# Performance work log

Measured on AMD Instinct MI355X. Metric: run time of the kernel, lower is better.

Reference implementation:

```python
import jax, jax.numpy as jnp
import numpy as np
import math

B, C, T = 32, 512, 1024
QUERY_DIM = 512
SCALE = 1.0 / math.sqrt(QUERY_DIM)


def setup_inputs() -> dict:
    key = jax.random.key(0)
    ks = jax.random.split(key, 10)
    lim = 1.0 / math.sqrt(C)  # torch Linear default init range
    return {
        "x": jax.random.normal(ks[0], (B, C, T), dtype=jnp.float32),
        "g_query": jax.random.uniform(ks[1], (B, C, T), dtype=jnp.float32),
        "g_keys": jax.random.uniform(ks[2], (B, C, T), dtype=jnp.float32),
        "g_values": jax.random.uniform(ks[3], (B, C, T), dtype=jnp.float32),
        "Wq": jax.random.uniform(ks[4], (C, C), jnp.float32, -lim, lim),
        "bq": jax.random.uniform(ks[5], (C,), jnp.float32, -lim, lim),
        "Wk": jax.random.uniform(ks[6], (C, C), jnp.float32, -lim, lim),
        "bk": jax.random.uniform(ks[7], (C,), jnp.float32, -lim, lim),
        "Wv": jax.random.uniform(ks[8], (C, C), jnp.float32, -lim, lim),
        "bv": jax.random.uniform(ks[9], (C,), jnp.float32, -lim, lim),
    }


def reference(x, g_query, g_keys, g_values, Wq, bq, Wk, bk, Wv, bv):
    # x, gates: [B, C, T] -> transpose to [B, T, C]
    xt = jnp.swapaxes(x, 1, 2)
    gq = jnp.swapaxes(g_query, 1, 2)
    gk = jnp.swapaxes(g_keys, 1, 2)
    gv = jnp.swapaxes(g_values, 1, 2)
    # torch Linear: y = x @ W^T + b
    q = gq * (jnp.einsum('btc,dc->btd', xt, Wq) + bq)  # [B, T, C]
    k = gk * (jnp.einsum('btc,dc->btd', xt, Wk) + bk)  # [B, T, C]
    v = gv * (jnp.einsum('btc,dc->btd', xt, Wv) + bv)  # [B, T, C]
    # energy[b,c,d] = sum_t q[b,t,c] * k[b,t,d]  (channel-channel attention)
    energy = jnp.einsum('btc,btd->bcd', q, k)  # [B, C, C]
    attn = jax.nn.softmax(energy * SCALE, axis=2)
    # out[b,c,t] = sum_d attn[b,c,d] * v[b,t,d]
    out = jnp.einsum('bcd,btd->bct', attn, v)  # [B, C, T]
    return out
```

## Files before the change

kernel.cpp:

```cpp
#include <hip/hip_runtime.h>
#include <math.h>


#define B_ 32
#define C_ 512
#define T_ 1024
#define TC_ ((size_t)524288)
#define CC_ ((size_t)262144)
#define SCALE_ 0.04419417382415922f

typedef short bf16x8 __attribute__((ext_vector_type(8)));
typedef float f32x4 __attribute__((ext_vector_type(4)));

__device__ __forceinline__ unsigned short f2b(float f) {
    unsigned int u = __float_as_uint(f);
    u += 0x7fff + ((u >> 16) & 1);
    return (unsigned short)(u >> 16);
}
__device__ __forceinline__ float b2f(unsigned short h) {
    return __uint_as_float(((unsigned int)h) << 16);
}

#define GLDS(gp, lp) __builtin_amdgcn_global_load_lds( \
    (const __attribute__((address_space(1))) unsigned int*)(const void*)(gp), \
    (__attribute__((address_space(3))) unsigned int*)(void*)(lp), 16, 0, 0)

template<int M, int N, int K, int LD, int EP>
__global__ __launch_bounds__(256, 2) void gemm_nt(
    const unsigned short* __restrict__ Ahi, const unsigned short* __restrict__ Alo, size_t sA,
    const unsigned short* __restrict__ Bhi, const unsigned short* __restrict__ Blo, size_t sB,
    float* __restrict__ Cf, size_t sCf,
    unsigned short* __restrict__ Chi, unsigned short* __restrict__ Clo, size_t sC,
    const float* __restrict__ gate, size_t sG,
    const float* __restrict__ bias)
{
    __shared__ __attribute__((aligned(16))) unsigned short sAh0[128 * 32];
    __shared__ __attribute__((aligned(16))) unsigned short sAl0[128 * 32];
    __shared__ __attribute__((aligned(16))) unsigned short sBh0[128 * 32];
    __shared__ __attribute__((aligned(16))) unsigned short sBl0[128 * 32];
    __shared__ __attribute__((aligned(16))) unsigned short sAh1[128 * 32];
    __shared__ __attribute__((aligned(16))) unsigned short sAl1[128 * 32];
    __shared__ __attribute__((aligned(16))) unsigned short sBh1[128 * 32];
    __shared__ __attribute__((aligned(16))) unsigned short sBl1[128 * 32];

    const int tid  = threadIdx.x;
    const int lane = tid & 63;
    const int wave = tid >> 6;
    const int bz   = (EP == 2) ? (blockIdx.z >> 1) : blockIdx.z;
    const size_t kbase = (EP == 2) ? (size_t)(blockIdx.z & 1) * K : 0;
    const int m0   = blockIdx.y * 128;
    const int n0   = blockIdx.x * 128;

    const unsigned short* pAh = Ahi + (size_t)bz * sA;
    const unsigned short* pAl = Alo + (size_t)bz * sA;
    const unsigned short* pBh = Bhi + (size_t)bz * sB;
    const unsigned short* pBl = Blo + (size_t)bz * sB;

    const int srow = wave * 32;
    const int lr   = lane >> 2;
    const int lk   = (lane & 3) * 8;
    const size_t gA0 = (size_t)(m0 + srow + lr) * LD + lk + kbase;
    const size_t gA1 = (size_t)(m0 + srow + 16 + lr) * LD + lk + kbase;
    const size_t gB0 = (size_t)(n0 + srow + lr) * LD + lk + kbase;
    const size_t gB1 = (size_t)(n0 + srow + 16 + lr) * LD + lk + kbase;

    const int wm = (wave & 1) * 64;
    const int wn = (wave >> 1) * 64;
    const int fr = lane & 15;
    const int fk = (lane >> 4) * 8;

    f32x4 acc[4][4] = {};

#define STAGE(AH, AL, BH, BL, koff) do { \
    GLDS(pAh + gA0 + (koff), &AH[srow * 32]); \
    GLDS(pAh + gA1 + (koff), &AH[(srow + 16) * 32]); \
    GLDS(pAl + gA0 + (koff), &AL[srow * 32]); \
    GLDS(pAl + gA1 + (koff), &AL[(srow + 16) * 32]); \
    GLDS(pBh + gB0 + (koff), &BH[srow * 32]); \
    GLDS(pBh + gB1 + (koff), &BH[(srow + 16) * 32]); \
    GLDS(pBl + gB0 + (koff), &BL[srow * 32]); \
    GLDS(pBl + gB1 + (koff), &BL[(srow + 16) * 32]); \
} while (0)

#define COMPUTE(AH, AL, BH, BL) do { \
    bf16x8 aH[4], aL[4], bH[4], bL[4]; \
    _Pragma("unroll") \
    for (int i = 0; i < 4; ++i) { \
        int ar = (wm + i * 16 + fr) * 32 + fk; \
        int br = (wn + i * 16 + fr) * 32 + fk; \
        aH[i] = *(const bf16x8*)(const void*)&AH[ar]; \
        aL[i] = *(const bf16x8*)(const void*)&AL[ar]; \
        bH[i] = *(const bf16x8*)(const void*)&BH[br]; \
        bL[i] = *(const bf16x8*)(const void*)&BL[br]; \
    } \
    _Pragma("unroll") \
    for (int mi = 0; mi < 4; ++mi) \
        _Pragma("unroll") \
        for (int ni = 0; ni < 4; ++ni) { \
            acc[mi][ni] = __builtin_amdgcn_mfma_f32_16x16x32_bf16(aL[mi], bH[ni], acc[mi][ni], 0, 0, 0); \
            acc[mi][ni] = __builtin_amdgcn_mfma_f32_16x16x32_bf16(aH[mi], bL[ni], acc[mi][ni], 0, 0, 0); \
            acc[mi][ni] = __builtin_amdgcn_mfma_f32_16x16x32_bf16(aH[mi], bH[ni], acc[mi][ni], 0, 0, 0); \
        } \
} while (0)

    STAGE(sAh0, sAl0, sBh0, sBl0, 0);
    __syncthreads();

    for (int k0 = 0; k0 < K; k0 += 64) {
        STAGE(sAh1, sAl1, sBh1, sBl1, k0 + 32);
        COMPUTE(sAh0, sAl0, sBh0, sBl0);
        __syncthreads();
        if (k0 + 64 < K) STAGE(sAh0, sAl0, sBh0, sBl0, k0 + 64);
        COMPUTE(sAh1, sAl1, sBh1, sBl1);
        __syncthreads();
    }

#undef STAGE
#undef COMPUTE

    #pragma unroll
    for (int mi = 0; mi < 4; ++mi) {
        #pragma unroll
        for (int r = 0; r < 4; ++r) {
            int m = m0 + wm + mi * 16 + (lane >> 4) * 4 + r;
            #pragma unroll
            for (int ni = 0; ni < 4; ++ni) {
                int n = n0 + wn + ni * 16 + fr;
                float v = acc[mi][ni][r];
                size_t idx = (size_t)m * N + n;
                if (EP == 0 || EP == 1) {
                    float g = gate[(size_t)bz * sG + idx];
                    float val = g * (v + bias[EP == 0 ? m : n]);
                    unsigned short h = f2b(val);
                    Chi[(size_t)bz * sC + idx] = h;
                    Clo[(size_t)bz * sC + idx] = f2b(val - b2f(h));
                } else if (EP == 2) {
                    Cf[(size_t)blockIdx.z * sCf + idx] = v * SCALE_;
                } else {
                    Cf[(size_t)bz * sCf + idx] = v;
                }
            }
        }
    }
}

__global__ __launch_bounds__(256) void transpose_split(
    const float* __restrict__ x, const float* __restrict__ gv,
    unsigned short* __restrict__ xThi, unsigned short* __restrict__ xTlo,
    float* __restrict__ gvT, int bc, int b_off)
{
    __shared__ float s[64][65];
    const int z = blockIdx.z;
    const int job = z / bc, bz = z % bc;
    const int t0 = blockIdx.x * 64, c0 = blockIdx.y * 64;
    const float* src = (job ? gv : x) + (size_t)(b_off + bz) * TC_;
    const int col = threadIdx.x & 63, rb = threadIdx.x >> 6;

    #pragma unroll
    for (int i = 0; i < 64; i += 4)
        s[i + rb][col] = src[(size_t)(c0 + i + rb) * T_ + t0 + col];
    __syncthreads();

    const size_t ob = (size_t)bz * TC_;
    #pragma unroll
    for (int i = 0; i < 64; i += 4) {
        int tr = i + rb;
        float v = s[col][tr];
        size_t o = ob + (size_t)(t0 + tr) * C_ + c0 + col;
        if (job == 0) {
            unsigned short h = f2b(v);
            xThi[o] = h;
            xTlo[o] = f2b(v - b2f(h));
        } else {
            gvT[o] = v;
        }
    }
}

__global__ __launch_bounds__(256) void split_mat(
    const float* __restrict__ W, unsigned short* __restrict__ hi,
    unsigned short* __restrict__ lo, int n)
{
    int i = blockIdx.x * 256 + threadIdx.x;
    if (i < n) {
        float v = W[i];
        unsigned short h = f2b(v);
        hi[i] = h;
        lo[i] = f2b(v - b2f(h));
    }
}

__global__ __launch_bounds__(256) void softmax_split(
    const float* __restrict__ E, unsigned short* __restrict__ Ahi,
    unsigned short* __restrict__ Alo)
{
    const int row = blockIdx.x;
    const int bz = row >> 9;
    const int c  = row & (C_ - 1);
    const float* p0 = E + (size_t)(2 * bz) * CC_ + (size_t)c * C_;
    const int tid = threadIdx.x;

    float v0 = p0[tid] + p0[CC_ + tid];
    float v1 = p0[tid + 256] + p0[CC_ + tid + 256];
    float m = fmaxf(v0, v1);
    #pragma unroll
    for (int off = 32; off > 0; off >>= 1)
        m = fmaxf(m, __shfl_down(m, off, 64));

    __shared__ float sm[4];
    if ((tid & 63) == 0) sm[tid >> 6] = m;
    __syncthreads();
    float M = fmaxf(fmaxf(sm[0], sm[1]), fmaxf(sm[2], sm[3]));

    float e0 = expf(v0 - M), e1 = expf(v1 - M);
    float s = e0 + e1;
    #pragma unroll
    for (int off = 32; off > 0; off >>= 1)
        s += __shfl_down(s, off, 64);

    __shared__ float ss[4];
    if ((tid & 63) == 0) ss[tid >> 6] = s;
    __syncthreads();
    float inv = 1.0f / (ss[0] + ss[1] + ss[2] + ss[3]);

    float a0 = e0 * inv, a1 = e1 * inv;
    size_t o = (size_t)row * C_ + tid;
    unsigned short h0 = f2b(a0);
    Ahi[o] = h0;  Alo[o] = f2b(a0 - b2f(h0));
    unsigned short h1 = f2b(a1);
    Ahi[o + 256] = h1;  Alo[o + 256] = f2b(a1 - b2f(h1));
}

extern "C" void kernel_launch(void* const* d_in, const int* in_sizes, int n_in,
                              void* d_out, int out_size, void* d_ws, size_t ws_size,
                              hipStream_t stream) {
    const float* x  = (const float*)d_in[0];
    const float* gq = (const float*)d_in[1];
    const float* gk = (const float*)d_in[2];
    const float* gv = (const float*)d_in[3];
    const float* Wq = (const float*)d_in[4];
    const float* bq = (const float*)d_in[5];
    const float* Wk = (const float*)d_in[6];
    const float* bk = (const float*)d_in[7];
    const float* Wv = (const float*)d_in[8];
    const float* bv = (const float*)d_in[9];
    float* out = (float*)d_out;

    const size_t wBytes = 6 * CC_ * 2;
    const size_t perBatch = 2 * TC_ * 2 + TC_ * 4 + 6 * TC_ * 2
                          + 2 * CC_ * 4 + 2 * CC_ * 2;
    int bc = 1;
    for (int cand = B_; cand >= 1; cand >>= 1)
        if (wBytes + (size_t)cand * perBatch <= ws_size) { bc = cand; break; }

    char* p = (char*)d_ws;
    auto take = [&](size_t bytes) { char* r = p; p += bytes; return r; };
    unsigned short* Wqh = (unsigned short*)take(CC_ * 2);
    unsigned short* Wql = (unsigned short*)take(CC_ * 2);
    unsigned short* Wkh = (unsigned short*)take(CC_ * 2);
    unsigned short* Wkl = (unsigned short*)take(CC_ * 2);
    unsigned short* Wvh = (unsigned short*)take(CC_ * 2);
    unsigned short* Wvl = (unsigned short*)take(CC_ * 2);
    unsigned short* xThi = (unsigned short*)take((size_t)bc * TC_ * 2);
    unsigned short* xTlo = (unsigned short*)take((size_t)bc * TC_ * 2);
    float*          gvT  = (float*)take((size_t)bc * TC_ * 4);
    unsigned short* Qh = (unsigned short*)take((size_t)bc * TC_ * 2);
    unsigned short* Ql = (unsigned short*)take((size_t)bc * TC_ * 2);
    unsigned short* Kh = (unsigned short*)take((size_t)bc * TC_ * 2);
    unsigned short* Kl = (unsigned short*)take((size_t)bc * TC_ * 2);
    unsigned short* Vh = (unsigned short*)take((size_t)bc * TC_ * 2);
    unsigned short* Vl = (unsigned short*)take((size_t)bc * TC_ * 2);
    float*          E  = (float*)take((size_t)bc * 2 * CC_ * 4);
    unsigned short* Ah = (unsigned short*)take((size_t)bc * CC_ * 2);
    unsigned short* Al = (unsigned short*)take((size_t)bc * CC_ * 2);

    dim3 blk(256);
    split_mat<<<(int)(CC_ / 256), blk, 0, stream>>>(Wq, Wqh, Wql, (int)CC_);
    split_mat<<<(int)(CC_ / 256), blk, 0, stream>>>(Wk, Wkh, Wkl, (int)CC_);
    split_mat<<<(int)(CC_ / 256), blk, 0, stream>>>(Wv, Wvh, Wvl, (int)CC_);

    for (int b_off = 0; b_off < B_; b_off += bc) {
        transpose_split<<<dim3(T_ / 64, C_ / 64, 2 * bc), blk, 0, stream>>>(
            x, gv, xThi, xTlo, gvT, bc, b_off);

        gemm_nt<512, 1024, 512, 512, 0><<<dim3(8, 4, bc), blk, 0, stream>>>(
            Wqh, Wql, 0, xThi, xTlo, TC_, nullptr, 0, Qh, Ql, TC_,
            gq + (size_t)b_off * TC_, TC_, bq);
        gemm_nt<512, 1024, 512, 512, 0><<<dim3(8, 4, bc), blk, 0, stream>>>(
            Wkh, Wkl, 0, xThi, xTlo, TC_, nullptr, 0, Kh, Kl, TC_,
            gk + (size_t)b_off * TC_, TC_, bk);
        gemm_nt<1024, 512, 512, 512, 1><<<dim3(4, 8, bc), blk, 0, stream>>>(
            xThi, xTlo, TC_, Wvh, Wvl, 0, nullptr, 0, Vh, Vl, TC_,
            gvT, TC_, bv);
        gemm_nt<512, 512, 512, 1024, 2><<<dim3(4, 4, 2 * bc), blk, 0, stream>>>(
            Qh, Ql, TC_, Kh, Kl, TC_, E, CC_, nullptr, nullptr, 0, nullptr, 0, nullptr);
        softmax_split<<<dim3(bc * C_), blk, 0, stream>>>(E, Ah, Al);
        gemm_nt<512, 1024, 512, 512, 3><<<dim3(8, 4, bc), blk, 0, stream>>>(
            Ah, Al, CC_, Vh, Vl, TC_, out + (size_t)b_off * TC_, TC_,
            nullptr, nullptr, 0, nullptr, 0, nullptr);
    }
}
```

Baseline: 679.7 us.

## Enlarge GEMM tiles to 256x128 with 8 waves, swizzled LDS, batch-interleaved 1D grid

The split-bf16 GEMM kernel now runs 512 threads per block on 256x128 output tiles, so each B fragment is reused across twice as many rows. The K offset in global loads is XOR-swizzled so fragment reads from LDS avoid bank conflicts, and the 3D grid becomes a 1D grid whose index mapping interleaves batches across groups of 8 blocks, likely to spread work over chiplets and keep shared weights in cache. The larger LDS footprint (about 96KB) probably caps occupancy at one block per CU, and there are fewer blocks per launch.

```diff
diff --git a/kernel.cpp b/kernel.cpp
--- a/kernel.cpp
+++ b/kernel.cpp
@@ -26,68 +26,81 @@
     (__attribute__((address_space(3))) unsigned int*)(void*)(lp), 16, 0, 0)
 
 template<int M, int N, int K, int LD, int EP>
-__global__ __launch_bounds__(256, 2) void gemm_nt(
+__global__ __launch_bounds__(512, 2) void gemm_nt(
     const unsigned short* __restrict__ Ahi, const unsigned short* __restrict__ Alo, size_t sA,
     const unsigned short* __restrict__ Bhi, const unsigned short* __restrict__ Blo, size_t sB,
     float* __restrict__ Cf, size_t sCf,
     unsigned short* __restrict__ Chi, unsigned short* __restrict__ Clo, size_t sC,
     const float* __restrict__ gate, size_t sG,
-    const float* __restrict__ bias)
+    const float* __restrict__ bias,
+    int nbatch)
 {
-    __shared__ __attribute__((aligned(16))) unsigned short sAh0[128 * 32];
-    __shared__ __attribute__((aligned(16))) unsigned short sAl0[128 * 32];
+    __shared__ __attribute__((aligned(16))) unsigned short sAh0[256 * 32];
+    __shared__ __attribute__((aligned(16))) unsigned short sAl0[256 * 32];
     __shared__ __attribute__((aligned(16))) unsigned short sBh0[128 * 32];
     __shared__ __attribute__((aligned(16))) unsigned short sBl0[128 * 32];
-    __shared__ __attribute__((aligned(16))) unsigned short sAh1[128 * 32];
-    __shared__ __attribute__((aligned(16))) unsigned short sAl1[128 * 32];
+    __shared__ __attribute__((aligned(16))) unsigned short sAh1[256 * 32];
+    __shared__ __attribute__((aligned(16))) unsigned short sAl1[256 * 32];
     __shared__ __attribute__((aligned(16))) unsigned short sBh1[128 * 32];
     __shared__ __attribute__((aligned(16))) unsigned short sBl1[128 * 32];
+
+    constexpr int GY = M / 256;
+    constexpr int GX = N / 128;
+    constexpr int TN = GY * GX;
 
     const int tid  = threadIdx.x;
     const int lane = tid & 63;
     const int wave = tid >> 6;
-    const int bz   = (EP == 2) ? (blockIdx.z >> 1) : blockIdx.z;
-    const size_t kbase = (EP == 2) ? (size_t)(blockIdx.z & 1) * K : 0;
-    const int m0   = blockIdx.y * 128;
-    const int n0   = blockIdx.x * 128;
+
+    const int ZU = (EP == 2) ? 2 * nbatch : nbatch;
+    const int l = blockIdx.x;
+    int tile, zu;
+    if ((ZU & 7) == 0) {
+        const int g = ZU >> 3;
+        const int r = l >> 3;
+        zu = (l & 7) + ((r % g) << 3);
+        tile = r / g;
+    } else { tile = l % TN; zu = l / TN; }
+    const int bz   = (EP == 2) ? (zu >> 1) : zu;
+    const size_t kbase = (EP == 2) ? (size_t)(zu & 1) * K : 0;
+    const int m0   = (tile / GX) * 256;
+    const int n0   = (tile % GX) * 128;
 
     const unsigned short* pAh = Ahi + (size_t)bz * sA;
     const unsigned short* pAl = Alo + (size_t)bz * sA;
     const unsigned short* pBh = Bhi + (size_t)bz * sB;
     const unsigned short* pBl = Blo + (size_t)bz * sB;
 
-    const int srow = wave * 32;
+    const int srowA = wave * 32;
+    const int srowB = wave * 16;
     const int lr   = lane >> 2;
-    const int lk   = (lane & 3) * 8;
-    const size_t gA0 = (size_t)(m0 + srow + lr) * LD + lk + kbase;
-    const size_t gA1 = (size_t)(m0 + srow + 16 + lr) * LD + lk + kbase;
-    const size_t gB0 = (size_t)(n0 + srow + lr) * LD + lk + kbase;
-    const size_t gB1 = (size_t)(n0 + srow + 16 + lr) * LD + lk + kbase;
-
-    const int wm = (wave & 1) * 64;
-    const int wn = (wave >> 1) * 64;
+    const int lk   = (((lane & 3) ^ ((lane >> 3) & 3)) * 8);
+    const size_t gA0 = (size_t)(m0 + srowA + lr) * LD + lk + kbase;
+    const size_t gA1 = gA0 + (size_t)16 * LD;
+    const size_t gB0 = (size_t)(n0 + srowB + lr) * LD + lk + kbase;
+
+    const int wm = (wave >> 1) * 64;
+    const int wn = (wave & 1) * 64;
     const int fr = lane & 15;
-    const int fk = (lane >> 4) * 8;
+    const int cSw = (((lane >> 4) ^ ((fr >> 1) & 3)) * 8);
 
     f32x4 acc[4][4] = {};
 
 #define STAGE(AH, AL, BH, BL, koff) do { \
-    GLDS(pAh + gA0 + (koff), &AH[srow * 32]); \
-    GLDS(pAh + gA1 + (koff), &AH[(srow + 16) * 32]); \
-    GLDS(pAl + gA0 + (koff), &AL[srow * 32]); \
-    GLDS(pAl + gA1 + (koff), &AL[(srow + 16) * 32]); \
-    GLDS(pBh + gB0 + (koff), &BH[srow * 32]); \
-    GLDS(pBh + gB1 + (koff), &BH[(srow + 16) * 32]); \
-    GLDS(pBl + gB0 + (koff), &BL[srow * 32]); \
-    GLDS(pBl + gB1 + (koff), &BL[(srow + 16) * 32]); \
+    GLDS(pAh + gA0 + (koff), &AH[srowA * 32]); \
+    GLDS(pAh + gA1 + (koff), &AH[(srowA + 16) * 32]); \
+    GLDS(pAl + gA0 + (koff), &AL[srowA * 32]); \
+    GLDS(pAl + gA1 + (koff), &AL[(srowA + 16) * 32]); \
+    GLDS(pBh + gB0 + (koff), &BH[srowB * 32]); \
+    GLDS(pBl + gB0 + (koff), &BL[srowB * 32]); \
 } while (0)
 
 #define COMPUTE(AH, AL, BH, BL) do { \
     bf16x8 aH[4], aL[4], bH[4], bL[4]; \
     _Pragma("unroll") \
     for (int i = 0; i < 4; ++i) { \
-        int ar = (wm + i * 16 + fr) * 32 + fk; \
-        int br = (wn + i * 16 + fr) * 32 + fk; \
+        int ar = (wm + i * 16 + fr) * 32 + cSw; \
+        int br = (wn + i * 16 + fr) * 32 + cSw; \
         aH[i] = *(const bf16x8*)(const void*)&AH[ar]; \
         aL[i] = *(const bf16x8*)(const void*)&AL[ar]; \
         bH[i] = *(const bf16x8*)(const void*)&BH[br]; \
@@ -135,7 +148,7 @@
                     Chi[(size_t)bz * sC + idx] = h;
                     Clo[(size_t)bz * sC + idx] = f2b(val - b2f(h));
                 } else if (EP == 2) {
-                    Cf[(size_t)blockIdx.z * sCf + idx] = v * SCALE_;
+                    Cf[(size_t)zu * sCf + idx] = v * SCALE_;
                 } else {
                     Cf[(size_t)bz * sCf + idx] = v;
                 }
@@ -275,6 +288,7 @@
     unsigned short* Al = (unsigned short*)take((size_t)bc * CC_ * 2);
 
     dim3 blk(256);
+    dim3 gblk(512);
     split_mat<<<(int)(CC_ / 256), blk, 0, stream>>>(Wq, Wqh, Wql, (int)CC_);
     split_mat<<<(int)(CC_ / 256), blk, 0, stream>>>(Wk, Wkh, Wkl, (int)CC_);
     split_mat<<<(int)(CC_ / 256), blk, 0, stream>>>(Wv, Wvh, Wvl, (int)CC_);
@@ -283,20 +297,20 @@
         transpose_split<<<dim3(T_ / 64, C_ / 64, 2 * bc), blk, 0, stream>>>(
             x, gv, xThi, xTlo, gvT, bc, b_off);
 
-        gemm_nt<512, 1024, 512, 512, 0><<<dim3(8, 4, bc), blk, 0, stream>>>(
+        gemm_nt<512, 1024, 512, 512, 0><<<dim3(16 * bc), gblk, 0, stream>>>(
             Wqh, Wql, 0, xThi, xTlo, TC_, nullptr, 0, Qh, Ql, TC_,
-            gq + (size_t)b_off * TC_, TC_, bq);
-        gemm_nt<512, 1024, 512, 512, 0><<<dim3(8, 4, bc), blk, 0, stream>>>(
+            gq + (size_t)b_off * TC_, TC_, bq, bc);
+        gemm_nt<512, 1024, 512, 512, 0><<<dim3(16 * bc), gblk, 0, stream>>>(
             Wkh, Wkl, 0, xThi, xTlo, TC_, nullptr, 0, Kh, Kl, TC_,
-            gk + (size_t)b_off * TC_, TC_, bk);
-        gemm_nt<1024, 512, 512, 512, 1><<<dim3(4, 8, bc), blk, 0, stream>>>(
+            gk + (size_t)b_off * TC_, TC_, bk, bc);
+        gemm_nt<1024, 512, 512, 512, 1><<<dim3(16 * bc), gblk, 0, stream>>>(
             xThi, xTlo, TC_, Wvh, Wvl, 0, nullptr, 0, Vh, Vl, TC_,
-            gvT, TC_, bv);
-        gemm_nt<512, 512, 512, 1024, 2><<<dim3(4, 4, 2 * bc), blk, 0, stream>>>(
-            Qh, Ql, TC_, Kh, Kl, TC_, E, CC_, nullptr, nullptr, 0, nullptr, 0, nullptr);
+            gvT, TC_, bv, bc);
+        gemm_nt<512, 512, 512, 1024, 2><<<dim3(16 * bc), gblk, 0, stream>>>(
+            Qh, Ql, TC_, Kh, Kl, TC_, E, CC_, nullptr, nullptr, 0, nullptr, 0, nullptr, bc);
         softmax_split<<<dim3(bc * C_), blk, 0, stream>>>(E, Ah, Al);
-        gemm_nt<512, 1024, 512, 512, 3><<<dim3(8, 4, bc), blk, 0, stream>>>(
+        gemm_nt<512, 1024, 512, 512, 3><<<dim3(16 * bc), gblk, 0, stream>>>(
             Ah, Al, CC_, Vh, Vl, TC_, out + (size_t)b_off * TC_, TC_,
-            nullptr, nullptr, 0, nullptr, 0, nullptr);
-    }
-}
+            nullptr, nullptr, 0, nullptr, 0, nullptr, bc);
+    }
+}
```

Measured after the change: 643.2 us. -5.4%, faster.
